# Kernel tuning notes

Hardware: AMD Instinct MI355X
Metric: run time of the kernel (lower is better)

## Reference

```python
import jax, jax.numpy as jnp
import numpy as np

N = 100000
E = 3200000
F_IN = 128
H = 16
NUM_GRAPHS = 1000


def gcn_conv(x, W, b, src, dst, norm, n_nodes):
    # x: [N, Fin] -> h: [N, Fout]; gather along src, scale, scatter-add to dst
    h = x @ W
    msg = h[src] * norm[:, None]            # [E_tot, Fout]
    out = jax.ops.segment_sum(msg, dst, num_segments=n_nodes)
    return out + b


def setup_inputs() -> dict:
    key = jax.random.key(0)
    k0, k1, k2, k3, k4, k5 = jax.random.split(key, 6)
    x = jax.random.normal(k0, (N, F_IN), dtype=jnp.float32)
    edge_index = jax.random.randint(k1, (2, E), 0, N, dtype=jnp.int64)
    batch = jnp.sort(jax.random.randint(k2, (N,), 0, NUM_GRAPHS, dtype=jnp.int64))
    # Glorot-style init for GCN weights, zero bias (PyG default)
    W1 = jax.random.normal(k3, (F_IN, H), dtype=jnp.float32) / np.sqrt(F_IN)
    b1 = jnp.zeros((H,), dtype=jnp.float32)
    W2 = jax.random.normal(k4, (H, 1), dtype=jnp.float32) / np.sqrt(H)
    b2 = jnp.zeros((1,), dtype=jnp.float32)
    return {"x": x, "edge_index": edge_index, "batch": batch,
            "W1": W1, "b1": b1, "W2": W2, "b2": b2}


def reference(x, edge_index, batch, W1, b1, W2, b2):
    n_nodes = x.shape[0]
    # add self-loops (PyG GCNConv default)
    loop = jnp.arange(n_nodes, dtype=edge_index.dtype)
    src = jnp.concatenate([edge_index[0], loop])
    dst = jnp.concatenate([edge_index[1], loop])
    # symmetric normalization D^{-1/2} (A+I) D^{-1/2}
    deg = jax.ops.segment_sum(jnp.ones_like(dst, dtype=x.dtype), dst,
                              num_segments=n_nodes)
    dinv = jnp.where(deg > 0, jax.lax.rsqrt(deg), 0.0)
    norm = dinv[src] * dinv[dst]            # [E_tot]

    h = gcn_conv(x, W1, b1, src, dst, norm, n_nodes)   # [N, 16]
    h = jax.nn.relu(h)
    h = gcn_conv(h, W2, b2, src, dst, norm, n_nodes)   # [N, 1]
    # global_add_pool over graphs
    out = jax.ops.segment_sum(h, batch, num_segments=NUM_GRAPHS)  # [G, 1]
    return out
```

## Files before the change

kernel.cpp:

```cpp
#include <hip/hip_runtime.h>

#define NB_MAX   512
#define CHUNK    8192
#define CAPB     16384
#define SORT_CAP 12288

__device__ inline unsigned short f2bf(float f) {
    unsigned u = __float_as_uint(f);
    u += 0x7FFFu + ((u >> 16) & 1u);
    return (unsigned short)(u >> 16);
}

__global__ void k_zero(float* __restrict__ out, int g, int* __restrict__ bcnt) {
    int t = blockIdx.x * blockDim.x + threadIdx.x;
    if (t < g) out[t] = 0.f;
    if (t < NB_MAX) bcnt[t] = 0;
}

__global__ __launch_bounds__(512) void k_scatter(const int* __restrict__ src,
                                                 const int* __restrict__ dst,
                                                 int* __restrict__ bcnt,
                                                 int* __restrict__ packed,
                                                 int E) {
    __shared__ int lh[NB_MAX];
    __shared__ int lscan[NB_MAX];
    __shared__ int ldelta[NB_MAX];
    __shared__ int sorted[CHUNK];
    __shared__ unsigned short sbkt[CHUNK];
    int t = threadIdx.x;
    int e0 = blockIdx.x * CHUNK;
    int e1 = min(e0 + CHUNK, E);
    int cnt = e1 - e0;
    lh[t] = 0;
    __syncthreads();
    for (int e = e0 + t; e < e1; e += 512) atomicAdd(&lh[dst[e] >> 8], 1);
    __syncthreads();
    int v = lh[t];
    lscan[t] = v;
    __syncthreads();
    for (int o = 1; o < 512; o <<= 1) {
        int u = (t >= o) ? lscan[t - o] : 0;
        __syncthreads();
        lscan[t] += u;
        __syncthreads();
    }
    int ex = lscan[t] - v;
    int gbase = v ? atomicAdd(&bcnt[t], v) : 0;
    lh[t] = ex;
    ldelta[t] = t * CAPB + gbase - ex;
    __syncthreads();
    for (int e = e0 + t; e < e1; e += 512) {
        int d = dst[e];
        int b = d >> 8;
        int r = atomicAdd(&lh[b], 1);
        sorted[r] = src[e] | ((d & 255) << 24);
        sbkt[r] = (unsigned short)b;
    }
    __syncthreads();
    for (int i = t; i < cnt; i += 512)
        packed[i + ldelta[sbkt[i]]] = sorted[i];
}

__global__ __launch_bounds__(512) void k_sortgemm(const int* __restrict__ packed,
                                                  const int* __restrict__ bcnt,
                                                  const float* __restrict__ x,
                                                  const float* __restrict__ W1,
                                                  int* __restrict__ sidx2,
                                                  int* __restrict__ noffs,
                                                  int* __restrict__ ndeg,
                                                  float* __restrict__ dinv,
                                                  unsigned short* __restrict__ hs,
                                                  int n) {
    __shared__ int hist[256];
    __shared__ int scan[256];
    __shared__ int curs[256];
    __shared__ float sdinv[256];
    __shared__ float sW[128 * 16];
    __shared__ __align__(16) char smem[SORT_CAP * 4];
    int* sorted = (int*)smem;
    float* sXT = (float*)smem;

    int t = threadIdx.x, b = blockIdx.x;
    int seg0 = b * CAPB, cnt = bcnt[b];
    int node0 = b << 8;

    for (int q = t; q < 2048; q += 512) sW[q] = W1[q];
    if (t < 256) hist[t] = 0;
    __syncthreads();
    for (int e = t; e < cnt; e += 512)
        atomicAdd(&hist[(unsigned)packed[seg0 + e] >> 24], 1);
    __syncthreads();
    int v = 0;
    if (t < 256) { v = hist[t]; scan[t] = v; }
    __syncthreads();
    for (int o = 1; o < 256; o <<= 1) {
        int u = (t < 256 && t >= o) ? scan[t - o] : 0;
        __syncthreads();
        if (t < 256) scan[t] += u;
        __syncthreads();
    }
    int ex = 0;
    if (t < 256) {
        ex = scan[t] - v;
        float di = rsqrtf((float)v + 1.0f);
        sdinv[t] = di;
        int node = node0 + t;
        if (node < n) {
            noffs[node] = seg0 + ex;
            ndeg[node] = v;
            dinv[node] = di;
        }
    }
    if (cnt <= SORT_CAP) {
        if (t < 256) curs[t] = ex;
        __syncthreads();
        for (int e = t; e < cnt; e += 512) {
            int p = packed[seg0 + e];
            int dl = (int)((unsigned)p >> 24);
            int r = atomicAdd(&curs[dl], 1);
            sorted[r] = p & 0xFFFFFF;
        }
        __syncthreads();
        for (int i = t; i < cnt; i += 512)
            sidx2[seg0 + i] = sorted[i];
    } else {
        if (t < 256) curs[t] = seg0 + ex;
        __syncthreads();
        for (int e = t; e < cnt; e += 512) {
            int p = packed[seg0 + e];
            int dl = (int)((unsigned)p >> 24);
            int r = atomicAdd(&curs[dl], 1);
            sidx2[r] = p & 0xFFFFFF;
        }
    }

    int ng = t >> 2, cg = t & 3;
    float acc[4][4];
#pragma unroll
    for (int i = 0; i < 4; i++)
#pragma unroll
        for (int j = 0; j < 4; j++) acc[i][j] = 0.f;
    for (int kc = 0; kc < 4; kc++) {
        __syncthreads();
#pragma unroll
        for (int pass = 0; pass < 4; pass++) {
            int row = pass * 64 + (t >> 3);
            int node = node0 + row;
            const float* xp = x + (size_t)min(node, n - 1) * 128 + kc * 32 + (t & 7) * 4;
            float4 vv = *(const float4*)xp;
            int k0 = (t & 7) * 4;
            sXT[(k0 + 0) * 260 + row] = vv.x;
            sXT[(k0 + 1) * 260 + row] = vv.y;
            sXT[(k0 + 2) * 260 + row] = vv.z;
            sXT[(k0 + 3) * 260 + row] = vv.w;
        }
        __syncthreads();
        if (t < 256) {
            const float* wbase = sW + kc * 32 * 16 + cg * 4;
#pragma unroll 8
            for (int k = 0; k < 32; k++) {
                float4 xv = *(const float4*)&sXT[k * 260 + ng * 4];
                float4 wv = *(const float4*)&wbase[k * 16];
                acc[0][0] += xv.x * wv.x; acc[0][1] += xv.x * wv.y;
                acc[0][2] += xv.x * wv.z; acc[0][3] += xv.x * wv.w;
                acc[1][0] += xv.y * wv.x; acc[1][1] += xv.y * wv.y;
                acc[1][2] += xv.y * wv.z; acc[1][3] += xv.y * wv.w;
                acc[2][0] += xv.z * wv.x; acc[2][1] += xv.z * wv.y;
                acc[2][2] += xv.z * wv.z; acc[2][3] += xv.z * wv.w;
                acc[3][0] += xv.w * wv.x; acc[3][1] += xv.w * wv.y;
                acc[3][2] += xv.w * wv.z; acc[3][3] += xv.w * wv.w;
            }
        }
    }
    if (t < 256) {
#pragma unroll
        for (int i = 0; i < 4; i++) {
            int local = ng * 4 + i;
            int node = node0 + local;
            if (node < n) {
                float di = sdinv[local];
                ushort4 o;
                o.x = f2bf(acc[i][0] * di);
                o.y = f2bf(acc[i][1] * di);
                o.z = f2bf(acc[i][2] * di);
                o.w = f2bf(acc[i][3] * di);
                *(ushort4*)&hs[(size_t)node * 16 + cg * 4] = o;
            }
        }
    }
}

#define UNPACK_ADD(u)                                        \
    acc[0] += __uint_as_float((u).x << 16);                  \
    acc[1] += __uint_as_float((u).x & 0xFFFF0000u);          \
    acc[2] += __uint_as_float((u).y << 16);                  \
    acc[3] += __uint_as_float((u).y & 0xFFFF0000u);          \
    acc[4] += __uint_as_float((u).z << 16);                  \
    acc[5] += __uint_as_float((u).z & 0xFFFF0000u);          \
    acc[6] += __uint_as_float((u).w << 16);                  \
    acc[7] += __uint_as_float((u).w & 0xFFFF0000u);

__global__ __launch_bounds__(256) void k_agg1(const uint4* __restrict__ hs4,
                                              const int* __restrict__ noffs,
                                              const int* __restrict__ ndeg,
                                              const int* __restrict__ sidx2,
                                              const float* __restrict__ dinv,
                                              const float* __restrict__ b1,
                                              const float* __restrict__ W2,
                                              float* __restrict__ hw, int n) {
    int tid = blockIdx.x * 256 + threadIdx.x;
    int node = tid >> 1, q = tid & 1;
    if (node >= n) return;
    float acc[8];
    uint4 u0 = hs4[(size_t)node * 2 + q];
    acc[0] = __uint_as_float(u0.x << 16);
    acc[1] = __uint_as_float(u0.x & 0xFFFF0000u);
    acc[2] = __uint_as_float(u0.y << 16);
    acc[3] = __uint_as_float(u0.y & 0xFFFF0000u);
    acc[4] = __uint_as_float(u0.z << 16);
    acc[5] = __uint_as_float(u0.z & 0xFFFF0000u);
    acc[6] = __uint_as_float(u0.w << 16);
    acc[7] = __uint_as_float(u0.w & 0xFFFF0000u);
    int e0 = noffs[node], e1 = e0 + ndeg[node];
    int e = e0;
    for (; e + 7 < e1; e += 8) {
        int s0 = sidx2[e],     s1 = sidx2[e + 1];
        int s2 = sidx2[e + 2], s3 = sidx2[e + 3];
        int s4 = sidx2[e + 4], s5 = sidx2[e + 5];
        int s6 = sidx2[e + 6], s7 = sidx2[e + 7];
        uint4 a0 = hs4[(size_t)s0 * 2 + q];
        uint4 a1 = hs4[(size_t)s1 * 2 + q];
        uint4 a2 = hs4[(size_t)s2 * 2 + q];
        uint4 a3 = hs4[(size_t)s3 * 2 + q];
        uint4 a4 = hs4[(size_t)s4 * 2 + q];
        uint4 a5 = hs4[(size_t)s5 * 2 + q];
        uint4 a6 = hs4[(size_t)s6 * 2 + q];
        uint4 a7 = hs4[(size_t)s7 * 2 + q];
        UNPACK_ADD(a0) UNPACK_ADD(a1) UNPACK_ADD(a2) UNPACK_ADD(a3)
        UNPACK_ADD(a4) UNPACK_ADD(a5) UNPACK_ADD(a6) UNPACK_ADD(a7)
    }
    for (; e < e1; e++) {
        uint4 a = hs4[(size_t)sidx2[e] * 2 + q];
        UNPACK_ADD(a)
    }
    float di = dinv[node];
    int base = q * 8;
    float r = 0.f;
#pragma unroll
    for (int j = 0; j < 8; j++)
        r += fmaxf(di * acc[j] + b1[base + j], 0.f) * W2[base + j];
    r += __shfl_down(r, 1, 2);
    if (q == 0) hw[node] = r * di;
}

__global__ __launch_bounds__(256) void k_agg2(const float* __restrict__ hw,
                                              const int* __restrict__ noffs,
                                              const int* __restrict__ ndeg,
                                              const int* __restrict__ sidx2,
                                              const float* __restrict__ dinv,
                                              const float* __restrict__ b2,
                                              const int* __restrict__ batch,
                                              float* __restrict__ out, int n) {
    __shared__ float v[128];
    __shared__ int g[128];
    int t = threadIdx.x;
    int tid = blockIdx.x * 256 + t;
    int i = tid >> 1, q = tid & 1;
    int li = t >> 1;
    float acc = 0.f;
    int gid = -1;
    if (i < n) {
        if (q == 0) acc = hw[i];
        int e0 = noffs[i], e1 = e0 + ndeg[i];
        int e = e0 + q;
        for (; e + 6 < e1; e += 8)
            acc += hw[sidx2[e]] + hw[sidx2[e + 2]] + hw[sidx2[e + 4]] + hw[sidx2[e + 6]];
        for (; e < e1; e += 2) acc += hw[sidx2[e]];
    }
    acc += __shfl_down(acc, 1, 2);
    if (i < n && q == 0) {
        v[li] = dinv[i] * acc + b2[0];
        g[li] = batch[i];
    } else if (q == 0) {
        v[li] = 0.f;
        g[li] = -1;
    }
    __syncthreads();
    if (q == 0) {
        int gid2 = g[li];
        if (gid2 >= 0 && (li == 0 || g[li - 1] != gid2)) {
            float s = v[li];
            for (int w = li + 1; w < 128 && g[w] == gid2; w++) s += v[w];
            atomicAdd(&out[gid2], s);
        }
    }
}

extern "C" void kernel_launch(void* const* d_in, const int* in_sizes, int n_in,
                              void* d_out, int out_size, void* d_ws, size_t ws_size,
                              hipStream_t stream) {
    int n = in_sizes[0] / 128;
    int E = in_sizes[1] / 2;
    const float* x     = (const float*)d_in[0];
    const int*   ei    = (const int*)d_in[1];
    const int*   src   = ei;
    const int*   dst   = ei + E;
    const int*   batch = (const int*)d_in[2];
    const float* W1    = (const float*)d_in[3];
    const float* b1    = (const float*)d_in[4];
    const float* W2    = (const float*)d_in[5];
    const float* b2    = (const float*)d_in[6];
    float* out = (float*)d_out;

    int nb = (n + 255) >> 8;

    char* p = (char*)d_ws;
    auto carve = [&](size_t bytes) {
        void* r = (void*)p;
        p += (bytes + 63) & ~(size_t)63;
        return r;
    };
    int*            bcnt   = (int*)carve(NB_MAX * 4);
    int*            packed = (int*)carve((size_t)nb * CAPB * 4);
    int*            sidx2  = (int*)carve((size_t)nb * CAPB * 4);
    int*            noffs  = (int*)carve((size_t)n * 4);
    int*            ndeg   = (int*)carve((size_t)n * 4);
    float*          dinv   = (float*)carve((size_t)n * 4);
    unsigned short* hs     = (unsigned short*)carve((size_t)n * 16 * 2);
    float*          hw     = (float*)carve((size_t)n * 4);

    k_zero<<<(out_size + 1023) / 1024, 1024, 0, stream>>>(out, out_size, bcnt);
    k_scatter<<<(E + CHUNK - 1) / CHUNK, 512, 0, stream>>>(src, dst, bcnt, packed, E);
    k_sortgemm<<<nb, 512, 0, stream>>>(packed, bcnt, x, W1, sidx2, noffs, ndeg,
                                       dinv, hs, n);
    k_agg1<<<((size_t)n * 2 + 255) / 256, 256, 0, stream>>>((const uint4*)hs, noffs, ndeg,
                                                            sidx2, dinv, b1, W2, hw, n);
    k_agg2<<<((size_t)n * 2 + 255) / 256, 256, 0, stream>>>(hw, noffs, ndeg, sidx2,
                                                            dinv, b2, batch, out, n);
}
```

Measured before the change: 120.9 us.

## Use wavefront shuffle scans, spread GEMM over all threads, add nontemporal loads

Replaces the shared-memory Hillis-Steele block scans in the scatter and sort kernels with wavefront shuffle scans plus a small per-wave sum array, which removes most of the block barriers. The sort+GEMM kernel now gives the 16-wide projection to all 512 threads, each computing 2 nodes instead of 4 with half the threads idle. Nontemporal loads are added for x and the sorted source indices in both aggregation passes so streamed data does not displace cached feature rows. The risk is lower per-thread register reuse in the GEMM, and the nontemporal hints may have no effect.

Measured after the change: 144.9 us. 1.2x slower.

```diff
diff --git a/kernel.cpp b/kernel.cpp
--- a/kernel.cpp
+++ b/kernel.cpp
@@ -23,8 +23,8 @@
                                                  int* __restrict__ packed,
                                                  int E) {
     __shared__ int lh[NB_MAX];
-    __shared__ int lscan[NB_MAX];
     __shared__ int ldelta[NB_MAX];
+    __shared__ int wsum[8];
     __shared__ int sorted[CHUNK];
     __shared__ unsigned short sbkt[CHUNK];
     int t = threadIdx.x;
@@ -36,15 +36,19 @@
     for (int e = e0 + t; e < e1; e += 512) atomicAdd(&lh[dst[e] >> 8], 1);
     __syncthreads();
     int v = lh[t];
-    lscan[t] = v;
-    __syncthreads();
-    for (int o = 1; o < 512; o <<= 1) {
-        int u = (t >= o) ? lscan[t - o] : 0;
-        __syncthreads();
-        lscan[t] += u;
-        __syncthreads();
-    }
-    int ex = lscan[t] - v;
+    int lane = t & 63, wid = t >> 6;
+    int s = v;
+#pragma unroll
+    for (int o = 1; o < 64; o <<= 1) {
+        int u = __shfl_up(s, o, 64);
+        if (lane >= o) s += u;
+    }
+    if (lane == 63) wsum[wid] = s;
+    __syncthreads();
+    int base = 0;
+#pragma unroll
+    for (int w = 0; w < 8; w++) base += (w < wid) ? wsum[w] : 0;
+    int ex = s + base - v;
     int gbase = v ? atomicAdd(&bcnt[t], v) : 0;
     lh[t] = ex;
     ldelta[t] = t * CAPB + gbase - ex;
@@ -72,8 +76,8 @@
                                                   unsigned short* __restrict__ hs,
                                                   int n) {
     __shared__ int hist[256];
-    __shared__ int scan[256];
     __shared__ int curs[256];
+    __shared__ int wsum[4];
     __shared__ float sdinv[256];
     __shared__ float sW[128 * 16];
     __shared__ __align__(16) char smem[SORT_CAP * 4];
@@ -90,18 +94,22 @@
     for (int e = t; e < cnt; e += 512)
         atomicAdd(&hist[(unsigned)packed[seg0 + e] >> 24], 1);
     __syncthreads();
-    int v = 0;
-    if (t < 256) { v = hist[t]; scan[t] = v; }
-    __syncthreads();
-    for (int o = 1; o < 256; o <<= 1) {
-        int u = (t < 256 && t >= o) ? scan[t - o] : 0;
-        __syncthreads();
-        if (t < 256) scan[t] += u;
-        __syncthreads();
-    }
+    int v = 0, s = 0;
+    if (t < 256) { v = hist[t]; s = v; }
+    int lane = t & 63, wid = t >> 6;
+#pragma unroll
+    for (int o = 1; o < 64; o <<= 1) {
+        int u = __shfl_up(s, o, 64);
+        if (lane >= o) s += u;
+    }
+    if (t < 256 && lane == 63) wsum[wid] = s;
+    __syncthreads();
     int ex = 0;
     if (t < 256) {
-        ex = scan[t] - v;
+        int base = 0;
+#pragma unroll
+        for (int w = 0; w < 4; w++) base += (w < wid) ? wsum[w] : 0;
+        ex = s + base - v;
         float di = rsqrtf((float)v + 1.0f);
         sdinv[t] = di;
         int node = node0 + t;
@@ -135,9 +143,9 @@
     }
 
     int ng = t >> 2, cg = t & 3;
-    float acc[4][4];
-#pragma unroll
-    for (int i = 0; i < 4; i++)
+    float acc[2][4];
+#pragma unroll
+    for (int i = 0; i < 2; i++)
 #pragma unroll
         for (int j = 0; j < 4; j++) acc[i][j] = 0.f;
     for (int kc = 0; kc < 4; kc++) {
@@ -147,7 +155,11 @@
             int row = pass * 64 + (t >> 3);
             int node = node0 + row;
             const float* xp = x + (size_t)min(node, n - 1) * 128 + kc * 32 + (t & 7) * 4;
-            float4 vv = *(const float4*)xp;
+            float4 vv;
+            vv.x = __builtin_nontemporal_load(xp);
+            vv.y = __builtin_nontemporal_load(xp + 1);
+            vv.z = __builtin_nontemporal_load(xp + 2);
+            vv.w = __builtin_nontemporal_load(xp + 3);
             int k0 = (t & 7) * 4;
             sXT[(k0 + 0) * 260 + row] = vv.x;
             sXT[(k0 + 1) * 260 + row] = vv.y;
@@ -155,37 +167,29 @@
             sXT[(k0 + 3) * 260 + row] = vv.w;
         }
         __syncthreads();
-        if (t < 256) {
-            const float* wbase = sW + kc * 32 * 16 + cg * 4;
+        const float* wbase = sW + kc * 32 * 16 + cg * 4;
 #pragma unroll 8
-            for (int k = 0; k < 32; k++) {
-                float4 xv = *(const float4*)&sXT[k * 260 + ng * 4];
-                float4 wv = *(const float4*)&wbase[k * 16];
-                acc[0][0] += xv.x * wv.x; acc[0][1] += xv.x * wv.y;
-                acc[0][2] += xv.x * wv.z; acc[0][3] += xv.x * wv.w;
-                acc[1][0] += xv.y * wv.x; acc[1][1] += xv.y * wv.y;
-                acc[1][2] += xv.y * wv.z; acc[1][3] += xv.y * wv.w;
-                acc[2][0] += xv.z * wv.x; acc[2][1] += xv.z * wv.y;
-                acc[2][2] += xv.z * wv.z; acc[2][3] += xv.z * wv.w;
-                acc[3][0] += xv.w * wv.x; acc[3][1] += xv.w * wv.y;
-                acc[3][2] += xv.w * wv.z; acc[3][3] += xv.w * wv.w;
-            }
-        }
-    }
-    if (t < 256) {
-#pragma unroll
-        for (int i = 0; i < 4; i++) {
-            int local = ng * 4 + i;
-            int node = node0 + local;
-            if (node < n) {
-                float di = sdinv[local];
-                ushort4 o;
-                o.x = f2bf(acc[i][0] * di);
-                o.y = f2bf(acc[i][1] * di);
-                o.z = f2bf(acc[i][2] * di);
-                o.w = f2bf(acc[i][3] * di);
-                *(ushort4*)&hs[(size_t)node * 16 + cg * 4] = o;
-            }
+        for (int k = 0; k < 32; k++) {
+            float2 xv = *(const float2*)&sXT[k * 260 + ng * 2];
+            float4 wv = *(const float4*)&wbase[k * 16];
+            acc[0][0] += xv.x * wv.x; acc[0][1] += xv.x * wv.y;
+            acc[0][2] += xv.x * wv.z; acc[0][3] += xv.x * wv.w;
+            acc[1][0] += xv.y * wv.x; acc[1][1] += xv.y * wv.y;
+            acc[1][2] += xv.y * wv.z; acc[1][3] += xv.y * wv.w;
+        }
+    }
+#pragma unroll
+    for (int i = 0; i < 2; i++) {
+        int local = ng * 2 + i;
+        int node = node0 + local;
+        if (node < n) {
+            float di = sdinv[local];
+            ushort4 o;
+            o.x = f2bf(acc[i][0] * di);
+            o.y = f2bf(acc[i][1] * di);
+            o.z = f2bf(acc[i][2] * di);
+            o.w = f2bf(acc[i][3] * di);
+            *(ushort4*)&hs[(size_t)node * 16 + cg * 4] = o;
         }
     }
 }
@@ -224,10 +228,14 @@
     int e0 = noffs[node], e1 = e0 + ndeg[node];
     int e = e0;
     for (; e + 7 < e1; e += 8) {
-        int s0 = sidx2[e],     s1 = sidx2[e + 1];
-        int s2 = sidx2[e + 2], s3 = sidx2[e + 3];
-        int s4 = sidx2[e + 4], s5 = sidx2[e + 5];
-        int s6 = sidx2[e + 6], s7 = sidx2[e + 7];
+        int s0 = __builtin_nontemporal_load(&sidx2[e]);
+        int s1 = __builtin_nontemporal_load(&sidx2[e + 1]);
+        int s2 = __builtin_nontemporal_load(&sidx2[e + 2]);
+        int s3 = __builtin_nontemporal_load(&sidx2[e + 3]);
+        int s4 = __builtin_nontemporal_load(&sidx2[e + 4]);
+        int s5 = __builtin_nontemporal_load(&sidx2[e + 5]);
+        int s6 = __builtin_nontemporal_load(&sidx2[e + 6]);
+        int s7 = __builtin_nontemporal_load(&sidx2[e + 7]);
         uint4 a0 = hs4[(size_t)s0 * 2 + q];
         uint4 a1 = hs4[(size_t)s1 * 2 + q];
         uint4 a2 = hs4[(size_t)s2 * 2 + q];
@@ -240,7 +248,7 @@
         UNPACK_ADD(a4) UNPACK_ADD(a5) UNPACK_ADD(a6) UNPACK_ADD(a7)
     }
     for (; e < e1; e++) {
-        uint4 a = hs4[(size_t)sidx2[e] * 2 + q];
+        uint4 a = hs4[(size_t)__builtin_nontemporal_load(&sidx2[e]) * 2 + q];
         UNPACK_ADD(a)
     }
     float di = dinv[node];
@@ -273,25 +281,32 @@
         if (q == 0) acc = hw[i];
         int e0 = noffs[i], e1 = e0 + ndeg[i];
         int e = e0 + q;
-        for (; e + 6 < e1; e += 8)
-            acc += hw[sidx2[e]] + hw[sidx2[e + 2]] + hw[sidx2[e + 4]] + hw[sidx2[e + 6]];
-        for (; e < e1; e += 2) acc += hw[sidx2[e]];
+        for (; e + 6 < e1; e += 8) {
+            int s0 = __builtin_nontemporal_load(&sidx2[e]);
+            int s1 = __builtin_nontemporal_load(&sidx2[e + 2]);
+            int s2 = __builtin_nontemporal_load(&sidx2[e + 4]);
+            int s3 = __builtin_nontemporal_load(&sidx2[e + 6]);
+            acc += hw[s0] + hw[s1] + hw[s2] + hw[s3];
+        }
+        for (; e < e1; e += 2) acc += hw[__builtin_nontemporal_load(&sidx2[e])];
     }
     acc += __shfl_down(acc, 1, 2);
-    if (i < n && q == 0) {
-        v[li] = dinv[i] * acc + b2[0];
-        g[li] = batch[i];
-    } else if (q == 0) {
-        v[li] = 0.f;
-        g[li] = -1;
+    if (q == 0) {
+        if (i < n) {
+            v[li] = dinv[i] * acc + b2[0];
+            g[li] = batch[i];
+        } else {
+            v[li] = 0.f;
+            g[li] = -1;
+        }
     }
     __syncthreads();
     if (q == 0) {
         int gid2 = g[li];
         if (gid2 >= 0 && (li == 0 || g[li - 1] != gid2)) {
-            float s = v[li];
-            for (int w = li + 1; w < 128 && g[w] == gid2; w++) s += v[w];
-            atomicAdd(&out[gid2], s);
+            float sum = v[li];
+            for (int w = li + 1; w < 128 && g[w] == gid2; w++) sum += v[w];
+            atomicAdd(&out[gid2], sum);
         }
     }
 }
```
